# Performance work log

Hardware: AMD Instinct MI355X
Metric: run time of the kernel (lower is better)

## Reference

```python
import jax, jax.numpy as jnp
import numpy as np

B, NPTS = 2, 60000
NX, NY = 256, 256
PCR0, PCR1 = -32.0, -32.0
PS0, PS1 = 0.25, 0.25
MAXPP = 32      # max points per pillar
MAXP = 12000    # max pillars
C = 64          # lidar_channels
SENT = NX * NY  # sentinel pillar id (> any valid id)
NEG = -1e9
EPS = 1e-5


def setup_inputs():
    key = jax.random.key(0)
    ks = jax.random.split(key, 16)
    xy = jax.random.uniform(ks[0], (B, NPTS, 2), minval=-34.0, maxval=34.0)
    z = jax.random.uniform(ks[1], (B, NPTS, 1), minval=-3.0, maxval=1.0)
    ir = jax.random.uniform(ks[2], (B, NPTS, 2))
    pts = jnp.concatenate([xy, z, ir], axis=-1).astype(jnp.float32)
    mask = jax.random.uniform(ks[3], (B, NPTS)) < 0.98

    def lin(k, i, o):
        return (jax.random.normal(k, (i, o)) / np.sqrt(i)).astype(jnp.float32)

    inp = {"lidar_points": pts, "lidar_mask": mask,
           "w1": lin(ks[4], 10, 64), "b1": 0.01 * jax.random.normal(ks[5], (64,), jnp.float32),
           "g1": jnp.ones(64, jnp.float32), "be1": jnp.zeros(64, jnp.float32),
           "w2": lin(ks[6], 64, 64), "b2": 0.01 * jax.random.normal(ks[7], (64,), jnp.float32),
           "g2": jnp.ones(64, jnp.float32), "be2": jnp.zeros(64, jnp.float32)}
    for i, n in enumerate(["1", "2", "3"]):
        inp["cw" + n] = (jax.random.normal(ks[8 + i], (64, 64, 3, 3)) / np.sqrt(64 * 9)).astype(jnp.float32)
        inp["cb" + n] = 0.01 * jax.random.normal(ks[11 + i], (64,), jnp.float32)
        inp["cg" + n] = jnp.ones(64, jnp.float32)
        inp["cbe" + n] = jnp.zeros(64, jnp.float32)
    return inp


def bn1d(x, g, b):  # training-mode BN over rows (biased var), matches torch BatchNorm1d forward
    m = x.mean(0)
    v = ((x - m) ** 2).mean(0)
    return (x - m) * jax.lax.rsqrt(v + EPS) * g + b


def bn2d(x, g, b):  # training-mode BN over (N,H,W) per channel
    m = x.mean((0, 2, 3), keepdims=True)
    v = ((x - m) ** 2).mean((0, 2, 3), keepdims=True)
    return (x - m) * jax.lax.rsqrt(v + EPS) * g[None, :, None, None] + b[None, :, None, None]


def conv3(x, w, b):
    y = jax.lax.conv_general_dilated(x, w, (1, 1), 'SAME',
                                     dimension_numbers=('NCHW', 'OIHW', 'NCHW'))
    return y + b[None, :, None, None]


def pillarize(pts, msk):
    """pts: (N,5) xyzir, msk: (N,) bool -> padded pillar tensors (fixed shapes)."""
    n = pts.shape[0]
    ix = jnp.clip(((pts[:, 0] - PCR0) / PS0).astype(jnp.int32), 0, NX - 1)
    iy = jnp.clip(((pts[:, 1] - PCR1) / PS1).astype(jnp.int32), 0, NY - 1)
    pid = jnp.where(msk, iy * NX + ix, SENT)
    # sorted unique ids; keep the first (smallest) MAXP, like torch.unique + truncation
    spid = jnp.sort(pid)
    is_new = jnp.concatenate([jnp.array([True]), spid[1:] != spid[:-1]])
    urank = jnp.cumsum(is_new) - 1
    dest = jnp.where(is_new & (urank < MAXP) & (spid < SENT), urank, MAXP)
    uids = jnp.full((MAXP + 1,), SENT, dtype=pid.dtype).at[dest].set(spid)[:MAXP]  # ascending, SENT-padded
    inv = jnp.clip(jnp.searchsorted(uids, pid), 0, MAXP - 1)
    valid = (uids[inv] == pid) & (pid < SENT)
    # rank of each point within its pillar, in original point order (stable sort)
    seg = jnp.where(valid, inv, MAXP)
    order = jnp.argsort(seg)  # stable
    sseg = seg[order]
    pos = jnp.arange(n)
    first = jnp.concatenate([jnp.array([True]), sseg[1:] != sseg[:-1]])
    start = jax.lax.cummax(jnp.where(first, pos, 0))
    rank = jnp.zeros(n, jnp.int32).at[order].set((pos - start).astype(jnp.int32))
    keep = valid & (rank < MAXPP)  # first MAXPP points per pillar (matches truncation-then-mean)
    seg2 = jnp.where(keep, inv, MAXP)  # dump slot = MAXP
    cnt = jnp.zeros(MAXP + 1, pts.dtype).at[seg2].add(1.0)
    sums = jnp.zeros((MAXP + 1, 3), pts.dtype).at[seg2].add(jnp.where(keep[:, None], pts[:, :3], 0.0))
    mean = sums / jnp.maximum(cnt, 1.0)[:, None]
    ctr = mean[seg2]  # per-point pillar centroid (over kept points)
    gx = PCR0 + ((pid % NX).astype(pts.dtype) + 0.5) * PS0
    gy = PCR1 + ((pid // NX).astype(pts.dtype) + 0.5) * PS1
    aug = jnp.concatenate([pts, pts[:, :3] - ctr, gx[:, None], gy[:, None]], axis=1)  # (N,10)
    rk = jnp.minimum(rank, MAXPP - 1)
    pf = jnp.zeros((MAXP + 1, MAXPP, 10), pts.dtype).at[seg2, rk].set(
        jnp.where(keep[:, None], aug, 0.0))[:MAXP]
    pm = jnp.zeros((MAXP + 1, MAXPP), bool).at[seg2, rk].set(keep)[:MAXP]
    pvalid = uids < SENT
    coords = jnp.where(pvalid[:, None], jnp.stack([uids % NX, uids // NX], axis=-1), 0)
    return pf, pm, coords, pvalid


def pillar_net(pf, pm, w1, b1, g1, be1, w2, b2, g2, be2):
    npil, pp, ci = pf.shape
    x = pf.reshape(npil * pp, ci) @ w1 + b1
    x = jax.nn.relu(bn1d(x, g1, be1))
    x = x @ w2 + b2
    x = jax.nn.relu(bn1d(x, g2, be2))
    x = x.reshape(npil, pp, -1)
    x = jnp.where(pm[:, :, None], x, NEG)
    return x.max(axis=1)  # (npil, C)


def reference(lidar_points, lidar_mask, w1, b1, g1, be1, w2, b2, g2, be2,
              cw1, cb1, cg1, cbe1, cw2, cb2, cg2, cbe2, cw3, cb3, cg3, cbe3):
    pf, pm, coords, pvalid = jax.vmap(pillarize)(lidar_points, lidar_mask)
    # pillar net is applied per batch element in the original loop -> per-sample BN stats
    feat = jax.vmap(lambda a, m: pillar_net(a, m, w1, b1, g1, be1, w2, b2, g2, be2))(pf, pm)
    lin = coords[..., 1] * NX + coords[..., 0]          # (B, MAXP)
    f = jnp.where(pvalid[..., None], feat, 0.0)          # padded pillars contribute nothing
    bev = jax.vmap(lambda l, ff: jnp.zeros((NY * NX, C), ff.dtype).at[l].add(ff))(lin, f)
    bev = bev.reshape(-1, NY, NX, C).transpose(0, 3, 1, 2)  # (B,C,NY,NX)
    x = jax.nn.relu(bn2d(conv3(bev, cw1, cb1), cg1, cbe1))
    x = jax.nn.relu(bn2d(conv3(x, cw2, cb2), cg2, cbe2))
    x = jax.nn.relu(bn2d(conv3(x, cw3, cb3), cg3, cbe3))
    return x
```

## Files before the change

kernel.cpp:

```cpp
#include <hip/hip_runtime.h>

#define NPTS 60000
#define NXG 256
#define NCELL 65536
#define MAXP 12000
#define MAXPP 32
#define NROWS (MAXP*MAXPP)

typedef float f32x32 __attribute__((ext_vector_type(32)));
typedef float f32x4  __attribute__((ext_vector_type(4)));
typedef short s16x8  __attribute__((ext_vector_type(8)));

__device__ __forceinline__ short to_bf16(float f){
  unsigned u = __float_as_uint(f);
  unsigned r = (u + 0x7FFFu + ((u>>16)&1u)) >> 16;
  return (short)r;
}
__device__ __forceinline__ float rl(float v, int c){
  return __int_as_float(__builtin_amdgcn_readlane(__float_as_int(v), c));
}

__global__ __launch_bounds__(256) void prep(uint4* __restrict__ p1, size_t n1,
                                            uint4* __restrict__ p2, size_t n2,
                                            const float* __restrict__ w0, const float* __restrict__ w1,
                                            const float* __restrict__ w2, short* __restrict__ wh){
  size_t idx = (size_t)blockIdx.x*256 + threadIdx.x;
  size_t stride = (size_t)gridDim.x*256;
  const uint4 z = make_uint4(0,0,0,0);
  for (size_t k=idx; k<n1; k+=stride) p1[k]=z;
  for (size_t k=idx; k<n2; k+=stride) p2[k]=z;
  for (size_t k=idx; k<3*36864; k+=stride){
    int l = (int)(k / 36864), r = (int)(k - (size_t)l*36864);
    const float* w = (l==0)? w0 : ((l==1)? w1 : w2);
    int ic = r & 63, oc = (r>>6)&63, tap = r>>12;
    wh[k] = to_bf16(w[(oc*64+ic)*9 + tap]);
  }
}

__global__ void compute_pid(const float* __restrict__ pts, const void* __restrict__ maskp,
                            int* __restrict__ pid, int* __restrict__ pptr,
                            int* __restrict__ ccnt){
  __shared__ int cf32, cbig;
  if (threadIdx.x==0){ cf32=0; cbig=0; }
  __syncthreads();
  {
    int lf=0, lb=0;
    const unsigned* mu = (const unsigned*)maskp;
    for (int k=0;k<4;k++){
      unsigned x = mu[threadIdx.x*4+k];
      if (x==0x3f800000u) lf++;
      else if (x>1u) lb++;
    }
    if (lf) atomicAdd(&cf32, lf);
    if (lb) atomicAdd(&cbig, lb);
  }
  __syncthreads();
  int mode = (cf32>64) ? 2 : ((cbig>0) ? 1 : 0);
  int i = blockIdx.x*blockDim.x + threadIdx.x;
  if (i>=NPTS) return;
  int b = blockIdx.y;
  int gi = b*NPTS+i;
  bool m;
  if (mode==0)      m = ((const int*)maskp)[gi]!=0;
  else if (mode==1) m = ((const unsigned char*)maskp)[gi]!=0;
  else              m = ((const float*)maskp)[gi]!=0.f;
  int cell = -1;
  if (m){
    float x = pts[(size_t)gi*5+0], y = pts[(size_t)gi*5+1];
    int ix = (int)((x - (-32.0f)) / 0.25f);
    ix = ix<0?0:(ix>255?255:ix);
    int iy = (int)((y - (-32.0f)) / 0.25f);
    iy = iy<0?0:(iy>255?255:iy);
    cell = iy*NXG + ix;
    atomicAdd(&ccnt[b*NCELL+cell], 1);
  }
  pid[gi] = cell;
  pptr[gi] = -1;
}

__global__ __launch_bounds__(256) void scan_a(const int* __restrict__ ccnt,
                                              int2* __restrict__ bpart){
  int b = blockIdx.y, blk = blockIdx.x, t = threadIdx.x;
  int4 v = *(const int4*)&ccnt[b*NCELL + blk*1024 + t*4];
  int occ = (v.x>0)+(v.y>0)+(v.z>0)+(v.w>0);
  int cnt = v.x+v.y+v.z+v.w;
  #pragma unroll
  for (int off=32; off>0; off>>=1){
    occ += __shfl_xor(occ, off, 64);
    cnt += __shfl_xor(cnt, off, 64);
  }
  __shared__ int so[4], sc[4];
  int wv = t>>6, lane = t&63;
  if (lane==0){ so[wv]=occ; sc[wv]=cnt; }
  __syncthreads();
  if (t==0) bpart[b*64+blk] = make_int2(so[0]+so[1]+so[2]+so[3], sc[0]+sc[1]+sc[2]+sc[3]);
}

__global__ __launch_bounds__(256) void scan_b(const int* __restrict__ ccnt,
    const int2* __restrict__ bpart,
    int* __restrict__ crank, int* __restrict__ cstart, int* __restrict__ pcell,
    int* __restrict__ misc, int* __restrict__ heavy){
  __shared__ int swo[4], swc[4], sk[4];
  __shared__ int bo_, bc_;
  int b = blockIdx.y, blk = blockIdx.x, t = threadIdx.x;
  int wv = t>>6, lane = t&63;
  if (t < 64){
    int2 p = bpart[b*64+t];
    int po = (t<blk)? p.x : 0;
    int pc = (t<blk)? p.y : 0;
    int to = p.x;
    int tc = p.y;
    #pragma unroll
    for (int off=32; off>0; off>>=1){
      po += __shfl_xor(po, off, 64);
      pc += __shfl_xor(pc, off, 64);
      to += __shfl_xor(to, off, 64);
      tc += __shfl_xor(tc, off, 64);
    }
    if (t==0){
      bo_ = po; bc_ = pc;
      if (blk==0){
        misc[1+b] = (to < MAXP) ? to : MAXP;
        misc[5+b] = tc;
      }
    }
  }
  int4 v = *(const int4*)&ccnt[b*NCELL + blk*1024 + t*4];
  int occ = (v.x>0)+(v.y>0)+(v.z>0)+(v.w>0);
  int cnt = v.x+v.y+v.z+v.w;
  int io = occ, ic = cnt;
  #pragma unroll
  for (int off=1; off<64; off<<=1){
    int ao = __shfl_up(io, off, 64);
    int ac = __shfl_up(ic, off, 64);
    if (lane >= off){ io += ao; ic += ac; }
  }
  if (lane==63){ swo[wv]=io; swc[wv]=ic; }
  __syncthreads();
  int wvo=0, wvc=0;
  #pragma unroll
  for (int w2=0; w2<4; w2++){
    if (w2<wv){ wvo += swo[w2]; wvc += swc[w2]; }
  }
  int eo = bo_ + wvo + io - occ;
  int ec = bc_ + wvc + ic - cnt;
  int kept = 0;
  int cellb = blk*1024 + t*4;
  int vv[4] = {v.x,v.y,v.z,v.w};
  #pragma unroll
  for (int j=0;j<4;j++){
    int c = cellb+j; int val = vv[j];
    if (val>0){
      crank[b*NCELL+c]=eo; cstart[b*NCELL+c]=ec;
      if (eo<MAXP){
        pcell[b*MAXP+eo]=c;
        kept += (val<MAXPP)? val : MAXPP;
        if (val>MAXPP){
          int hi = atomicAdd(&heavy[b],1);
          if (hi<64) heavy[2 + b*64 + hi] = c;
        }
      }
      eo++; ec+=val;
    }
  }
  #pragma unroll
  for (int off=32; off>0; off>>=1) kept += __shfl_xor(kept, off, 64);
  if (lane==0) sk[wv]=kept;
  __syncthreads();
  if (t==0) atomicAdd(&misc[3+b], sk[0]+sk[1]+sk[2]+sk[3]);
}

__global__ void scatter_points(const int* __restrict__ pid, const int* __restrict__ ccnt,
    const int* __restrict__ crank, const int* __restrict__ cstart,
    int* __restrict__ ctmp, int* __restrict__ plist, int* __restrict__ pptr){
  int i = blockIdx.x*blockDim.x + threadIdx.x;
  if (i>=NPTS) return;
  int b = blockIdx.y;
  int gi = b*NPTS+i;
  int cell = pid[gi];
  if (cell<0) return;
  int bc = b*NCELL+cell;
  int pos = cstart[bc] + atomicAdd(&ctmp[bc],1);
  plist[b*NPTS+pos] = i;
  int r = crank[bc];
  if (r>=0 && r<MAXP && ccnt[bc]<=MAXPP) pptr[gi] = r;
}

__global__ void heavy_select(const int* __restrict__ ccnt, const int* __restrict__ crank,
    const int* __restrict__ cstart, const int* __restrict__ plist,
    const int* __restrict__ heavy, int* __restrict__ pptr){
  int b = blockIdx.y;
  int hn = heavy[b]; if (hn>64) hn=64;
  if ((int)blockIdx.x >= hn) return;
  int cell = heavy[2 + b*64 + blockIdx.x];
  int bc = b*NCELL+cell;
  int cnt = ccnt[bc], start = cstart[bc], pr = crank[bc];
  for (int e=threadIdx.x; e<cnt; e+=blockDim.x){
    int pe = plist[b*NPTS+start+e];
    int rank=0;
    for (int k=0;k<cnt;k++) rank += (plist[b*NPTS+start+k] < pe);
    if (rank<MAXPP) pptr[b*NPTS+pe] = pr;
  }
}

__global__ __launch_bounds__(256) void gather_cpts(const float* __restrict__ pts,
    const int* __restrict__ pid, const int* __restrict__ pptr,
    const int* __restrict__ plist, const int* __restrict__ misc,
    float* __restrict__ cpts, float* __restrict__ psum){
  int pos = blockIdx.x*256 + threadIdx.x;
  int b = blockIdx.y;
  if (pos >= misc[5+b]) return;
  int i = plist[b*NPTS+pos];
  int gi = b*NPTS+i;
  const float* qp = &pts[(size_t)gi*5];
  float x=qp[0], y=qp[1], z=qp[2], i1=qp[3], i2=qp[4];
  int cell = pid[gi];
  int rid = pptr[gi];
  float gx = -32.0f + ((float)(cell&255)+0.5f)*0.25f;
  float gy = -32.0f + ((float)(cell>>8)+0.5f)*0.25f;
  float4* cp = (float4*)&cpts[(size_t)(b*NPTS+pos)*8];
  cp[0] = make_float4(x,y,z,i1);
  cp[1] = make_float4(i2,gx,gy,__int_as_float(rid));
  if (rid>=0){
    float* s = &psum[(size_t)(b*MAXP+rid)*4];
    atomicAdd(s+0,x); atomicAdd(s+1,y); atomicAdd(s+2,z); atomicAdd(s+3,1.f);
  }
}

#define MM_ACC(K,V) { if ((K)<32) m0[(K)&31]+=(V); else if ((K)<64) m1[((K)-32)&31]+=(V); else m2+=(V); }
__global__ __launch_bounds__(256) void moments(const float* __restrict__ cpts,
    const float* __restrict__ psum, const int* __restrict__ misc,
    float* __restrict__ lstat){
  int b = blockIdx.y;
  int n = misc[5+b];
  f32x32 m0, m1; float m2 = 0.f;
  #pragma unroll
  for (int j=0;j<32;j++){ m0[j]=0.f; m1[j]=0.f; }
  for (int pos = blockIdx.x*256+threadIdx.x; pos<n; pos += gridDim.x*256){
    const float4* cp = (const float4*)&cpts[(size_t)(b*NPTS+pos)*8];
    float4 f1 = cp[0], f2 = cp[1];
    int rid = __float_as_int(f2.w);
    if (rid<0) continue;
    float4 mc = *(const float4*)&psum[(size_t)(b*MAXP+rid)*4];
    float inv = 1.f/fmaxf(mc.w,1.f);
    float aug[10] = {f1.x,f1.y,f1.z,f1.w,f2.x,
                     f1.x-mc.x*inv, f1.y-mc.y*inv, f1.z-mc.z*inv, f2.y, f2.z};
    #pragma unroll
    for (int d=0; d<10; d++){
      #pragma unroll
      for (int e=d; e<10; e++){
        const int k = d*10 - d*(d-1)/2 + (e-d);
        MM_ACC(k, aug[d]*aug[e]);
      }
      const int kl = 55+d;
      MM_ACC(kl, aug[d]);
    }
  }
  int lane = threadIdx.x & 63;
  int rep = ((blockIdx.x*256+threadIdx.x)>>6) & 15;
  float* dst = &lstat[(size_t)(rep*2+b)*65];
  #pragma unroll
  for (int j=0;j<32;j++){
    float v = m0[j];
    #pragma unroll
    for (int off=32; off>0; off>>=1) v += __shfl_xor(v, off, 64);
    if (lane==0) atomicAdd(&dst[j], v);
  }
  #pragma unroll
  for (int j=0;j<32;j++){
    float v = m1[j];
    #pragma unroll
    for (int off=32; off>0; off>>=1) v += __shfl_xor(v, off, 64);
    if (lane==0) atomicAdd(&dst[32+j], v);
  }
  {
    float v = m2;
    #pragma unroll
    for (int off=32; off>0; off>>=1) v += __shfl_xor(v, off, 64);
    if (lane==0) atomicAdd(&dst[64], v);
  }
}

__global__ __launch_bounds__(256) void pillar_mlp(const float* __restrict__ cpts,
    const int* __restrict__ pcell, const int* __restrict__ cstart,
    const int* __restrict__ ccnt, const float* __restrict__ psum,
    const int* __restrict__ misc,
    const float* __restrict__ w1, const float* __restrict__ b1,
    const float* __restrict__ g1, const float* __restrict__ be1,
    const float* __restrict__ w2, const float* __restrict__ b2,
    const float* __restrict__ lstat, float* __restrict__ l2stat,
    float* __restrict__ fmx, float* __restrict__ fmn){
  __shared__ float sM[2][65];
  const int lane = threadIdx.x & 63;
  float w1c[10];
  #pragma unroll
  for (int d=0;d<10;d++) w1c[d] = w1[d*64+lane];
  for (int e=threadIdx.x; e<130; e+=256){
    int bb = e/65, k = e-bb*65;
    float s=0.f;
    for (int r=0;r<16;r++) s += lstat[(size_t)(r*2+bb)*65+k];
    sM[bb][k]=s;
  }
  __syncthreads();
  const float b1c = b1[lane], b2c = b2[lane];
  const float g1c = g1[lane], be1c = be1[lane];
  float sc1_0, sh1_0, sc1_1, sh1_1;
  #pragma unroll
  for (int bb=0;bb<2;bb++){
    float nk = (float)misc[3+bb];
    const float N = (float)NROWS;
    float pad = N - nk;
    float lw = 0.f;
    #pragma unroll
    for (int d=0;d<10;d++) lw += sM[bb][55+d]*w1c[d];
    float s = nk*b1c + lw;
    float qq = nk*b1c*b1c + 2.f*b1c*lw;
    #pragma unroll
    for (int d=0; d<10; d++){
      #pragma unroll
      for (int e=d; e<10; e++){
        float m = sM[bb][d*10 - d*(d-1)/2 + (e-d)];
        qq += ((d==e)?1.f:2.f)*m*w1c[d]*w1c[e];
      }
    }
    float St = s + pad*b1c;
    float Qt = qq + pad*b1c*b1c;
    float mu = St/N;
    float var = fmaxf(Qt/N - mu*mu, 0.f);
    float sc = g1c*rsqrtf(var+1e-5f);
    float sh = be1c-mu*sc;
    if (bb){ sc1_1=sc; sh1_1=sh; } else { sc1_0=sc; sh1_0=sh; }
  }
  f32x32 w2lo, w2hi;
  #pragma unroll
  for (int c=0;c<32;c++) w2lo[c] = w2[(size_t)c*64+lane];
  #pragma unroll
  for (int c=0;c<32;c++) w2hi[c] = w2[(size_t)(c+32)*64+lane];
  const int npil0 = misc[1], npil1 = misc[2];
  float s2_0=0.f, q2_0=0.f, s2_1=0.f, q2_1=0.f;

  const int wglobal = (blockIdx.x*256 + threadIdx.x) >> 6;
  const int nwaves = (gridDim.x*256) >> 6;
  for (int qq = wglobal; qq < 2*MAXP; qq += nwaves){
    int b = (qq >= MAXP) ? 1 : 0;
    int p = qq - b*MAXP;
    int npil = b ? npil1 : npil0;
    if (p >= npil) continue;
    int cell = pcell[b*MAXP+p];
    int bc = b*NCELL+cell;
    int cnt = ccnt[bc], start = cstart[bc];
    const float* mc = &psum[(size_t)(b*MAXP+p)*4];
    float minv = 1.f/fmaxf(mc[3],1.f);
    float mx = mc[0]*minv, my = mc[1]*minv, mz = mc[2]*minv;
    float gx = -32.0f + ((float)(cell&255)+0.5f)*0.25f;
    float gy = -32.0f + ((float)(cell>>8)+0.5f)*0.25f;
    float sc1 = b ? sc1_1 : sc1_0;
    float sh1 = b ? sh1_1 : sh1_0;
    float tmax = -1e30f, tmin = 1e30f;
    float s2 = 0.f, q2 = 0.f;
    const float4* cpb = (const float4*)&cpts[(size_t)(b*NPTS+start)*8];
    float4 f1 = cpb[0], f2 = cpb[1];
    for (int k=0; k<cnt; k++){
      float4 nf1, nf2;
      if (k+1 < cnt){ nf1 = cpb[2*(k+1)]; nf2 = cpb[2*(k+1)+1]; }
      int rid = __float_as_int(f2.w);
      if (rid == p){
        float x=f1.x, y=f1.y, z=f1.z, i1=f1.w, i2=f2.x;
        float acc = b1c;
        acc = fmaf(x, w1c[0], acc);
        acc = fmaf(y, w1c[1], acc);
        acc = fmaf(z, w1c[2], acc);
        acc = fmaf(i1, w1c[3], acc);
        acc = fmaf(i2, w1c[4], acc);
        acc = fmaf(x-mx, w1c[5], acc);
        acc = fmaf(y-my, w1c[6], acc);
        acc = fmaf(z-mz, w1c[7], acc);
        acc = fmaf(gx, w1c[8], acc);
        acc = fmaf(gy, w1c[9], acc);
        float zz = fmaxf(acc*sc1+sh1, 0.f);
        float t0 = b2c, t1 = 0.f, t2c = 0.f, t3 = 0.f;
        #pragma unroll
        for (int c=0;c<16;c++){
          t0  = fmaf(rl(zz,c),    w2lo[c],    t0);
          t1  = fmaf(rl(zz,c+16), w2lo[c+16], t1);
          t2c = fmaf(rl(zz,c+32), w2hi[c],    t2c);
          t3  = fmaf(rl(zz,c+48), w2hi[c+16], t3);
        }
        float t = (t0+t1)+(t2c+t3);
        tmax = fmaxf(tmax, t);
        tmin = fminf(tmin, t);
        s2 += t; q2 += t*t;
      }
      f1 = nf1; f2 = nf2;
    }
    fmx[(size_t)(b*MAXP+p)*64 + lane] = tmax;
    fmn[(size_t)(b*MAXP+p)*64 + lane] = tmin;
    if (b){ s2_1 += s2; q2_1 += q2; } else { s2_0 += s2; q2_0 += q2; }
  }
  int rep = wglobal & 15;
  atomicAdd(&l2stat[((rep*2+0)*2+0)*64+lane], s2_0);
  atomicAdd(&l2stat[((rep*2+0)*2+1)*64+lane], q2_0);
  atomicAdd(&l2stat[((rep*2+1)*2+0)*64+lane], s2_1);
  atomicAdd(&l2stat[((rep*2+1)*2+1)*64+lane], q2_1);
}

__global__ void stats_fin2(const float* __restrict__ w1, const float* __restrict__ b1,
    const float* __restrict__ g1, const float* __restrict__ be1,
    const float* __restrict__ w2, const float* __restrict__ b2,
    const float* __restrict__ g2, const float* __restrict__ be2,
    const float* __restrict__ lstat, const float* __restrict__ l2stat,
    const int* __restrict__ misc, float* __restrict__ stats){
  __shared__ float M[65];
  __shared__ float z0s[64];
  int b = blockIdx.x, c = threadIdx.x;
  for (int e=c; e<65; e+=64){
    float s=0.f;
    for (int r=0;r<16;r++) s += lstat[(size_t)(r*2+b)*65+e];
    M[e]=s;
  }
  __syncthreads();
  float wcol[10];
  #pragma unroll
  for (int d=0;d<10;d++) wcol[d] = w1[d*64+c];
  float b1c = b1[c];
  float nk = (float)misc[3+b];
  const float N = (float)NROWS;
  float pad = N - nk;
  float lw = 0.f;
  #pragma unroll
  for (int d=0;d<10;d++) lw += M[55+d]*wcol[d];
  float s = nk*b1c + lw;
  float qq = nk*b1c*b1c + 2.f*b1c*lw;
  #pragma unroll
  for (int d=0; d<10; d++){
    #pragma unroll
    for (int e=d; e<10; e++){
      float m = M[d*10 - d*(d-1)/2 + (e-d)];
      qq += ((d==e)?1.f:2.f)*m*wcol[d]*wcol[e];
    }
  }
  float St = s + pad*b1c;
  float Qt = qq + pad*b1c*b1c;
  float mu = St/N;
  float var = fmaxf(Qt/N - mu*mu, 0.f);
  float sc1 = g1[c]*rsqrtf(var+1e-5f);
  float sh1 = be1[c]-mu*sc1;
  float z0 = fmaxf(b1c*sc1+sh1, 0.f);
  z0s[c]=z0;
  __syncthreads();
  float t0 = b2[c];
  for (int i2=0;i2<64;i2++) t0 += z0s[i2]*w2[(size_t)i2*64+c];
  float s2 = pad*t0, q2 = pad*t0*t0;
  for (int r=0;r<16;r++){
    s2 += l2stat[((r*2+b)*2+0)*64+c];
    q2 += l2stat[((r*2+b)*2+1)*64+c];
  }
  float m2 = s2/N;
  float v2 = fmaxf(q2/N - m2*m2, 0.f);
  float sc2 = g2[c]*rsqrtf(v2+1e-5f);
  float* S = &stats[(size_t)b*512];
  S[384+c]=sc2; S[448+c]=be2[c]-m2*sc2;
}

__global__ void scatter_bev(const float* __restrict__ fmx, const float* __restrict__ fmn,
                            const int* __restrict__ pcell, const int* __restrict__ misc,
                            const float* __restrict__ stats, short* __restrict__ bevh){
  int tid = blockIdx.x*256+threadIdx.x;
  if (tid >= 2*64*MAXP) return;
  int c = tid & 63;
  int bp = tid >> 6;
  int b = bp / MAXP;
  int p = bp - b*MAXP;
  if (p >= misc[1+b]) return;
  float sc2 = stats[(size_t)b*512+384+c], sh2 = stats[(size_t)b*512+448+c];
  float t = (sc2 >= 0.f) ? fmx[tid] : fmn[tid];
  float v = fmaxf(sc2*t+sh2, 0.f);
  int cell = pcell[b*MAXP+p];
  bevh[((size_t)((b<<16) + cell))*64 + c] = to_bf16(v);
}

#define MFMA16(A,B,C) __builtin_amdgcn_mfma_f32_16x16x32_bf16(A,B,C,0,0,0)

__global__ __launch_bounds__(512,4) void conv_mfma(const short* __restrict__ xh,
    const short* __restrict__ wh, const float* __restrict__ bias,
    const float* __restrict__ pstat, const float* __restrict__ pg, const float* __restrict__ pbe,
    short* __restrict__ outh, float* __restrict__ outf,
    float* __restrict__ stat){
  __shared__ short sX[324*40];
  __shared__ short sW[576*40];
  __shared__ float sBN[128];
  __shared__ float ss[64], sq[64];
  const int tX = blockIdx.x*16, tY = blockIdx.y*16;
  const int b = blockIdx.z;
  const int t = threadIdx.x;
  const int lane = t & 63, wv = t >> 6;
  const int colx = lane & 15;
  const int kb = (lane >> 4) * 8;
  const int ocb = (wv >> 2) * 32;
  const int ry  = (wv & 3) * 4;
  if (t < 64){ ss[t]=0.f; sq[t]=0.f; }
  if (t >= 64 && t < 128 && pstat){
    int c = t-64;
    const float n = 131072.f;
    float m = pstat[c]/n;
    float v = fmaxf(pstat[64+c]/n - m*m, 0.f);
    float sc = pg[c]*rsqrtf(v+1e-5f);
    sBN[c]=sc; sBN[64+c]=pbe[c]-m*sc;
  }

  f32x4 a00={0.f,0.f,0.f,0.f}, a01=a00, a02=a00, a03=a00;
  f32x4 a10=a00, a11=a00, a12=a00, a13=a00;

  for (int h=0; h<2; ++h){
    __syncthreads();
    for (int e=t; e<1296; e+=512){
      int px = e>>2, j = e&3;
      int yy = px/18, xx = px - yy*18;
      int gy = tY+yy-1, gx = tX+xx-1;
      uint4 v = make_uint4(0,0,0,0);
      if ((unsigned)gy<256u && (unsigned)gx<256u){
        v = *(const uint4*)&xh[((size_t)((b<<16) + (gy<<8) + gx))*64 + h*32 + j*8];
        if (pstat){
          unsigned arr[4] = {v.x, v.y, v.z, v.w};
          #pragma unroll
          for (int j2=0;j2<4;j2++){
            unsigned wrd = arr[j2];
            int ch = h*32 + j*8 + j2*2;
            float lo = __uint_as_float(wrd<<16);
            float hi = __uint_as_float(wrd & 0xffff0000u);
            lo = fmaxf(lo*sBN[ch]+sBN[64+ch], 0.f);
            hi = fmaxf(hi*sBN[ch+1]+sBN[64+ch+1], 0.f);
            arr[j2] = (unsigned)(unsigned short)to_bf16(lo) |
                      (((unsigned)(unsigned short)to_bf16(hi))<<16);
          }
          v = make_uint4(arr[0],arr[1],arr[2],arr[3]);
        }
      }
      *(uint4*)&sX[px*40 + j*8] = v;
    }
    for (int e=t; e<2304; e+=512){
      int row = e>>2, j = e&3;
      int tap = row>>6, oc = row&63;
      uint4 v = *(const uint4*)&wh[(size_t)tap*4096 + oc*64 + h*32 + j*8];
      *(uint4*)&sW[row*40 + j*8] = v;
    }
    __syncthreads();
    #pragma unroll
    for (int tap=0; tap<9; ++tap){
      const int dy = tap/3, dx = tap - dy*3;
      s16x8 wA = *(const s16x8*)&sW[(tap*64 + ocb +  0 + colx)*40 + kb];
      s16x8 wB = *(const s16x8*)&sW[(tap*64 + ocb + 16 + colx)*40 + kb];
      s16x8 x0 = *(const s16x8*)&sX[((ry+0+dy)*18 + colx+dx)*40 + kb];
      s16x8 x1 = *(const s16x8*)&sX[((ry+1+dy)*18 + colx+dx)*40 + kb];
      s16x8 x2 = *(const s16x8*)&sX[((ry+2+dy)*18 + colx+dx)*40 + kb];
      s16x8 x3 = *(const s16x8*)&sX[((ry+3+dy)*18 + colx+dx)*40 + kb];
      a00 = MFMA16(wA,x0,a00); a01 = MFMA16(wA,x1,a01);
      a02 = MFMA16(wA,x2,a02); a03 = MFMA16(wA,x3,a03);
      a10 = MFMA16(wB,x0,a10); a11 = MFMA16(wB,x1,a11);
      a12 = MFMA16(wB,x2,a12); a13 = MFMA16(wB,x3,a13);
    }
  }
  const int ocl = (lane>>4)*4;
  #define DOG(G, A0,A1,A2,A3) { \
    const int oc0g = ocb + G*16 + ocl; \
    float bj0=bias[oc0g], bj1=bias[oc0g+1], bj2=bias[oc0g+2], bj3=bias[oc0g+3]; \
    float v00=A0[0]+bj0, v01=A0[1]+bj1, v02=A0[2]+bj2, v03=A0[3]+bj3; \
    float v10=A1[0]+bj0, v11=A1[1]+bj1, v12=A1[2]+bj2, v13=A1[3]+bj3; \
    float v20=A2[0]+bj0, v21=A2[1]+bj1, v22=A2[2]+bj2, v23=A2[3]+bj3; \
    float v30=A3[0]+bj0, v31=A3[1]+bj1, v32=A3[2]+bj2, v33=A3[3]+bj3; \
    float s0=v00+v10+v20+v30, q0=v00*v00+v10*v10+v20*v20+v30*v30; \
    float s1=v01+v11+v21+v31, q1=v01*v01+v11*v11+v21*v21+v31*v31; \
    float s2=v02+v12+v22+v32, q2=v02*v02+v12*v12+v22*v22+v32*v32; \
    float s3=v03+v13+v23+v33, q3=v03*v03+v13*v13+v23*v23+v33*v33; \
    s0+=__shfl_xor(s0,1,64); s0+=__shfl_xor(s0,2,64); s0+=__shfl_xor(s0,4,64); s0+=__shfl_xor(s0,8,64); \
    q0+=__shfl_xor(q0,1,64); q0+=__shfl_xor(q0,2,64); q0+=__shfl_xor(q0,4,64); q0+=__shfl_xor(q0,8,64); \
    s1+=__shfl_xor(s1,1,64); s1+=__shfl_xor(s1,2,64); s1+=__shfl_xor(s1,4,64); s1+=__shfl_xor(s1,8,64); \
    q1+=__shfl_xor(q1,1,64); q1+=__shfl_xor(q1,2,64); q1+=__shfl_xor(q1,4,64); q1+=__shfl_xor(q1,8,64); \
    s2+=__shfl_xor(s2,1,64); s2+=__shfl_xor(s2,2,64); s2+=__shfl_xor(s2,4,64); s2+=__shfl_xor(s2,8,64); \
    q2+=__shfl_xor(q2,1,64); q2+=__shfl_xor(q2,2,64); q2+=__shfl_xor(q2,4,64); q2+=__shfl_xor(q2,8,64); \
    s3+=__shfl_xor(s3,1,64); s3+=__shfl_xor(s3,2,64); s3+=__shfl_xor(s3,4,64); s3+=__shfl_xor(s3,8,64); \
    q3+=__shfl_xor(q3,1,64); q3+=__shfl_xor(q3,2,64); q3+=__shfl_xor(q3,4,64); q3+=__shfl_xor(q3,8,64); \
    if (colx==0){ \
      atomicAdd(&ss[oc0g],s0);   atomicAdd(&sq[oc0g],q0); \
      atomicAdd(&ss[oc0g+1],s1); atomicAdd(&sq[oc0g+1],q1); \
      atomicAdd(&ss[oc0g+2],s2); atomicAdd(&sq[oc0g+2],q2); \
      atomicAdd(&ss[oc0g+3],s3); atomicAdd(&sq[oc0g+3],q3); \
    } \
    if (outh){ \
      size_t pb = (size_t)((b<<16) + tX + colx); \
      *(short4*)&outh[(pb + ((tY+ry+0)<<8))*64 + oc0g] = make_short4(to_bf16(v00),to_bf16(v01),to_bf16(v02),to_bf16(v03)); \
      *(short4*)&outh[(pb + ((tY+ry+1)<<8))*64 + oc0g] = make_short4(to_bf16(v10),to_bf16(v11),to_bf16(v12),to_bf16(v13)); \
      *(short4*)&outh[(pb + ((tY+ry+2)<<8))*64 + oc0g] = make_short4(to_bf16(v20),to_bf16(v21),to_bf16(v22),to_bf16(v23)); \
      *(short4*)&outh[(pb + ((tY+ry+3)<<8))*64 + oc0g] = make_short4(to_bf16(v30),to_bf16(v31),to_bf16(v32),to_bf16(v33)); \
    } else { \
      size_t cb0 = (((size_t)(b*64+oc0g))<<16) + ((tY+ry)<<8) + tX + colx; \
      outf[cb0          ] = v00; outf[cb0+(1<<16)      ] = v01; outf[cb0+(2<<16)      ] = v02; outf[cb0+(3<<16)      ] = v03; \
      outf[cb0+256      ] = v10; outf[cb0+(1<<16)+256  ] = v11; outf[cb0+(2<<16)+256  ] = v12; outf[cb0+(3<<16)+256  ] = v13; \
      outf[cb0+512      ] = v20; outf[cb0+(1<<16)+512  ] = v21; outf[cb0+(2<<16)+512  ] = v22; outf[cb0+(3<<16)+512  ] = v23; \
      outf[cb0+768      ] = v30; outf[cb0+(1<<16)+768  ] = v31; outf[cb0+(2<<16)+768  ] = v32; outf[cb0+(3<<16)+768  ] = v33; \
    } \
  }
  DOG(0, a00,a01,a02,a03)
  DOG(1, a10,a11,a12,a13)
  #undef DOG
  __syncthreads();
  if (t < 64){
    atomicAdd(&stat[t],    ss[t]);
    atomicAdd(&stat[64+t], sq[t]);
  }
}

__global__ __launch_bounds__(256) void bn_apply(float* __restrict__ x, const float* __restrict__ bnst,
                                                const float* __restrict__ g, const float* __restrict__ be){
  __shared__ float sBN[128];
  if (threadIdx.x < 64){
    int c = threadIdx.x;
    const float n = 131072.f;
    float m = bnst[c]/n;
    float v = fmaxf(bnst[64+c]/n - m*m, 0.f);
    float sc = g[c]*rsqrtf(v+1e-5f);
    sBN[c]=sc; sBN[64+c]=be[c]-m*sc;
  }
  __syncthreads();
  size_t idx = (size_t)blockIdx.x*256 + threadIdx.x;
  size_t stride = (size_t)gridDim.x*256;
  float4* p = (float4*)x;
  for (size_t k=idx; k<2097152ULL; k+=stride){
    int c = (int)((k>>14)&63);
    float sc = sBN[c], sh = sBN[64+c];
    float4 v = p[k];
    v.x=fmaxf(v.x*sc+sh,0.f); v.y=fmaxf(v.y*sc+sh,0.f);
    v.z=fmaxf(v.z*sc+sh,0.f); v.w=fmaxf(v.w*sc+sh,0.f);
    p[k]=v;
  }
}

extern "C" void kernel_launch(void* const* d_in, const int* in_sizes, int n_in,
                              void* d_out, int out_size, void* d_ws, size_t ws_size,
                              hipStream_t stream){
  const float* pts  = (const float*)d_in[0];
  const void*  mask = d_in[1];
  const float* w1 = (const float*)d_in[2];
  const float* b1 = (const float*)d_in[3];
  const float* g1 = (const float*)d_in[4];
  const float* be1= (const float*)d_in[5];
  const float* w2 = (const float*)d_in[6];
  const float* b2 = (const float*)d_in[7];
  const float* g2 = (const float*)d_in[8];
  const float* be2= (const float*)d_in[9];
  const float* cw[3]  = {(const float*)d_in[10],(const float*)d_in[14],(const float*)d_in[18]};
  const float* cb[3]  = {(const float*)d_in[11],(const float*)d_in[15],(const float*)d_in[19]};
  const float* cg[3]  = {(const float*)d_in[12],(const float*)d_in[16],(const float*)d_in[20]};
  const float* cbe[3] = {(const float*)d_in[13],(const float*)d_in[17],(const float*)d_in[21]};
  float* out = (float*)d_out;

  char* W = (char*)d_ws;
  size_t off = 0;
  auto A = [&](size_t n){ size_t r = off; off = (off + n + 255) & ~(size_t)255; return r; };
  short*    BIGH  = (short*)   (W + A((size_t)2*NCELL*64*2));
  short*    OUT1H = (short*)   (W + A((size_t)2*NCELL*64*2));
  int*      PID   = (int*)     (W + A((size_t)2*NPTS*4));
  int*      CRANK = (int*)     (W + A((size_t)2*NCELL*4));
  int*      CSTART= (int*)     (W + A((size_t)2*NCELL*4));
  int*      PLIST = (int*)     (W + A((size_t)2*NPTS*4));
  int*      PPTR  = (int*)     (W + A((size_t)2*NPTS*4));
  int*      PCELL = (int*)     (W + A((size_t)2*MAXP*4));
  float*    CPTS  = (float*)   (W + A((size_t)2*NPTS*8*4));
  float*    FMX   = (float*)   (W + A((size_t)2*MAXP*64*4));
  float*    FMN   = (float*)   (W + A((size_t)2*MAXP*64*4));
  short*    WH    = (short*)   (W + A((size_t)3*36864*2));
  int2*     BPART = (int2*)    (W + A((size_t)2*64*8));
  size_t zbeg = off;
  int*      CCNT  = (int*)     (W + A((size_t)2*NCELL*4));
  int*      CTMP  = (int*)     (W + A((size_t)2*NCELL*4));
  float*    PSUM  = (float*)   (W + A((size_t)2*MAXP*16));
  float*    STATS = (float*)   (W + A((size_t)2*512*4));
  float*    LSTAT = (float*)   (W + A((size_t)16*2*65*4));
  float*    L2STAT= (float*)   (W + A((size_t)16*2*2*64*4));
  float*    BNST  = (float*)   (W + A((size_t)3*256*4));
  int*      HEAVY = (int*)     (W + A((size_t)(2+2*64)*4));
  int*      MISC  = (int*)     (W + A(256));
  size_t zend = off;

  prep<<<2048,256,0,stream>>>((uint4*)BIGH, (size_t)2*NCELL*64*2/16,
                              (uint4*)(W+zbeg), (zend-zbeg)/16,
                              cw[0], cw[1], cw[2], WH);

  dim3 perPt((NPTS+255)/256, 2);

  compute_pid<<<perPt,256,0,stream>>>(pts, mask, PID, PPTR, CCNT);
  scan_a<<<dim3(64,2),256,0,stream>>>(CCNT, BPART);
  scan_b<<<dim3(64,2),256,0,stream>>>(CCNT, BPART, CRANK, CSTART, PCELL, MISC, HEAVY);
  scatter_points<<<perPt,256,0,stream>>>(PID, CCNT, CRANK, CSTART, CTMP, PLIST, PPTR);
  heavy_select<<<dim3(64,2),64,0,stream>>>(CCNT, CRANK, CSTART, PLIST, HEAVY, PPTR);
  gather_cpts<<<perPt,256,0,stream>>>(pts, PID, PPTR, PLIST, MISC, CPTS, PSUM);
  moments<<<dim3(120,2),256,0,stream>>>(CPTS, PSUM, MISC, LSTAT);
  pillar_mlp<<<2048,256,0,stream>>>(CPTS, PCELL, CSTART, CCNT, PSUM, MISC,
                                    w1, b1, g1, be1, w2, b2, LSTAT, L2STAT, FMX, FMN);
  stats_fin2<<<2,64,0,stream>>>(w1, b1, g1, be1, w2, b2, g2, be2, LSTAT, L2STAT, MISC, STATS);
  scatter_bev<<<(2*64*MAXP+255)/256,256,0,stream>>>(FMX, FMN, PCELL, MISC, STATS, BIGH);

  conv_mfma<<<dim3(16,16,2),512,0,stream>>>(BIGH, WH, cb[0], nullptr, nullptr, nullptr,
                                            OUT1H, nullptr, BNST);
  conv_mfma<<<dim3(16,16,2),512,0,stream>>>(OUT1H, WH+36864, cb[1], BNST, cg[0], cbe[0],
                                            BIGH, nullptr, BNST+256);
  conv_mfma<<<dim3(16,16,2),512,0,stream>>>(BIGH, WH+2*36864, cb[2], BNST+256, cg[1], cbe[1],
                                            nullptr, out, BNST+512);
  bn_apply<<<2048,256,0,stream>>>(out, BNST+512, cg[2], cbe[2]);
}
```

Measured before the change: 217.6 us.

## Give each wave a contiguous pillar range and cache centroid offsets in point records

The moments kernel now writes each point's offset from its pillar mean into a widened 12-float point record, so pillar_mlp no longer reads psum. pillar_mlp is launched with a batch grid dimension, and each wave streams through a contiguous range of pillars' points, flushing max/min whenever the pillar id changes. Previously each wave handled one pillar at a time with per-pillar setup. The aim is to cut per-pillar overhead and improve load balance. The cost is extra point-record bandwidth and a possible imbalance when pillar point counts are uneven.

```diff
diff --git a/kernel.cpp b/kernel.cpp
--- a/kernel.cpp
+++ b/kernel.cpp
@@ -218,7 +218,7 @@
   int rid = pptr[gi];
   float gx = -32.0f + ((float)(cell&255)+0.5f)*0.25f;
   float gy = -32.0f + ((float)(cell>>8)+0.5f)*0.25f;
-  float4* cp = (float4*)&cpts[(size_t)(b*NPTS+pos)*8];
+  float4* cp = (float4*)&cpts[(size_t)(b*NPTS+pos)*12];
   cp[0] = make_float4(x,y,z,i1);
   cp[1] = make_float4(i2,gx,gy,__int_as_float(rid));
   if (rid>=0){
@@ -228,7 +228,7 @@
 }
 
 #define MM_ACC(K,V) { if ((K)<32) m0[(K)&31]+=(V); else if ((K)<64) m1[((K)-32)&31]+=(V); else m2+=(V); }
-__global__ __launch_bounds__(256) void moments(const float* __restrict__ cpts,
+__global__ __launch_bounds__(256) void moments(float* __restrict__ cpts,
     const float* __restrict__ psum, const int* __restrict__ misc,
     float* __restrict__ lstat){
   int b = blockIdx.y;
@@ -237,14 +237,15 @@
   #pragma unroll
   for (int j=0;j<32;j++){ m0[j]=0.f; m1[j]=0.f; }
   for (int pos = blockIdx.x*256+threadIdx.x; pos<n; pos += gridDim.x*256){
-    const float4* cp = (const float4*)&cpts[(size_t)(b*NPTS+pos)*8];
+    float4* cp = (float4*)&cpts[(size_t)(b*NPTS+pos)*12];
     float4 f1 = cp[0], f2 = cp[1];
     int rid = __float_as_int(f2.w);
     if (rid<0) continue;
     float4 mc = *(const float4*)&psum[(size_t)(b*MAXP+rid)*4];
     float inv = 1.f/fmaxf(mc.w,1.f);
-    float aug[10] = {f1.x,f1.y,f1.z,f1.w,f2.x,
-                     f1.x-mc.x*inv, f1.y-mc.y*inv, f1.z-mc.z*inv, f2.y, f2.z};
+    float dx = f1.x-mc.x*inv, dy = f1.y-mc.y*inv, dz = f1.z-mc.z*inv;
+    cp[2] = make_float4(dx,dy,dz,0.f);
+    float aug[10] = {f1.x,f1.y,f1.z,f1.w,f2.x, dx,dy,dz, f2.y,f2.z};
     #pragma unroll
     for (int d=0; d<10; d++){
       #pragma unroll
@@ -283,43 +284,40 @@
 
 __global__ __launch_bounds__(256) void pillar_mlp(const float* __restrict__ cpts,
     const int* __restrict__ pcell, const int* __restrict__ cstart,
-    const int* __restrict__ ccnt, const float* __restrict__ psum,
-    const int* __restrict__ misc,
+    const int* __restrict__ ccnt, const int* __restrict__ misc,
     const float* __restrict__ w1, const float* __restrict__ b1,
     const float* __restrict__ g1, const float* __restrict__ be1,
     const float* __restrict__ w2, const float* __restrict__ b2,
     const float* __restrict__ lstat, float* __restrict__ l2stat,
     float* __restrict__ fmx, float* __restrict__ fmn){
-  __shared__ float sM[2][65];
+  __shared__ float sM[65];
+  const int b = blockIdx.y;
   const int lane = threadIdx.x & 63;
   float w1c[10];
   #pragma unroll
   for (int d=0;d<10;d++) w1c[d] = w1[d*64+lane];
-  for (int e=threadIdx.x; e<130; e+=256){
-    int bb = e/65, k = e-bb*65;
+  for (int e=threadIdx.x; e<65; e+=256){
     float s=0.f;
-    for (int r=0;r<16;r++) s += lstat[(size_t)(r*2+bb)*65+k];
-    sM[bb][k]=s;
+    for (int r=0;r<16;r++) s += lstat[(size_t)(r*2+b)*65+e];
+    sM[e]=s;
   }
   __syncthreads();
   const float b1c = b1[lane], b2c = b2[lane];
-  const float g1c = g1[lane], be1c = be1[lane];
-  float sc1_0, sh1_0, sc1_1, sh1_1;
-  #pragma unroll
-  for (int bb=0;bb<2;bb++){
-    float nk = (float)misc[3+bb];
+  float sc1, sh1;
+  {
+    float nk = (float)misc[3+b];
     const float N = (float)NROWS;
     float pad = N - nk;
     float lw = 0.f;
     #pragma unroll
-    for (int d=0;d<10;d++) lw += sM[bb][55+d]*w1c[d];
+    for (int d=0;d<10;d++) lw += sM[55+d]*w1c[d];
     float s = nk*b1c + lw;
     float qq = nk*b1c*b1c + 2.f*b1c*lw;
     #pragma unroll
     for (int d=0; d<10; d++){
       #pragma unroll
       for (int e=d; e<10; e++){
-        float m = sM[bb][d*10 - d*(d-1)/2 + (e-d)];
+        float m = sM[d*10 - d*(d-1)/2 + (e-d)];
         qq += ((d==e)?1.f:2.f)*m*w1c[d]*w1c[e];
       }
     }
@@ -327,81 +325,82 @@
     float Qt = qq + pad*b1c*b1c;
     float mu = St/N;
     float var = fmaxf(Qt/N - mu*mu, 0.f);
-    float sc = g1c*rsqrtf(var+1e-5f);
-    float sh = be1c-mu*sc;
-    if (bb){ sc1_1=sc; sh1_1=sh; } else { sc1_0=sc; sh1_0=sh; }
+    sc1 = g1[lane]*rsqrtf(var+1e-5f);
+    sh1 = be1[lane]-mu*sc1;
   }
   f32x32 w2lo, w2hi;
   #pragma unroll
   for (int c=0;c<32;c++) w2lo[c] = w2[(size_t)c*64+lane];
   #pragma unroll
   for (int c=0;c<32;c++) w2hi[c] = w2[(size_t)(c+32)*64+lane];
-  const int npil0 = misc[1], npil1 = misc[2];
-  float s2_0=0.f, q2_0=0.f, s2_1=0.f, q2_1=0.f;
-
-  const int wglobal = (blockIdx.x*256 + threadIdx.x) >> 6;
-  const int nwaves = (gridDim.x*256) >> 6;
-  for (int qq = wglobal; qq < 2*MAXP; qq += nwaves){
-    int b = (qq >= MAXP) ? 1 : 0;
-    int p = qq - b*MAXP;
-    int npil = b ? npil1 : npil0;
-    if (p >= npil) continue;
-    int cell = pcell[b*MAXP+p];
-    int bc = b*NCELL+cell;
-    int cnt = ccnt[bc], start = cstart[bc];
-    const float* mc = &psum[(size_t)(b*MAXP+p)*4];
-    float minv = 1.f/fmaxf(mc[3],1.f);
-    float mx = mc[0]*minv, my = mc[1]*minv, mz = mc[2]*minv;
-    float gx = -32.0f + ((float)(cell&255)+0.5f)*0.25f;
-    float gy = -32.0f + ((float)(cell>>8)+0.5f)*0.25f;
-    float sc1 = b ? sc1_1 : sc1_0;
-    float sh1 = b ? sh1_1 : sh1_0;
+  const int npil = misc[1+b];
+  const int w = blockIdx.x*4 + (threadIdx.x>>6);
+  const int nw = gridDim.x*4;
+  float s2 = 0.f, q2 = 0.f;
+  const int ppw = (npil + nw - 1)/nw;
+  int p0 = w*ppw;
+  if (npil > 0 && p0 < npil){
+    int p1 = p0+ppw; if (p1>npil) p1=npil;
+    int c0 = pcell[b*MAXP+p0];
+    int cl = pcell[b*MAXP+p1-1];
+    int start = cstart[b*NCELL+c0];
+    int end = cstart[b*NCELL+cl] + ccnt[b*NCELL+cl];
+    int cur = -1;
     float tmax = -1e30f, tmin = 1e30f;
-    float s2 = 0.f, q2 = 0.f;
-    const float4* cpb = (const float4*)&cpts[(size_t)(b*NPTS+start)*8];
-    float4 f1 = cpb[0], f2 = cpb[1];
-    for (int k=0; k<cnt; k++){
-      float4 nf1, nf2;
-      if (k+1 < cnt){ nf1 = cpb[2*(k+1)]; nf2 = cpb[2*(k+1)+1]; }
-      int rid = __float_as_int(f2.w);
-      if (rid == p){
-        float x=f1.x, y=f1.y, z=f1.z, i1=f1.w, i2=f2.x;
+    const float4* cpb = (const float4*)&cpts[(size_t)b*NPTS*12];
+    float4 a0 = cpb[(size_t)start*3+0];
+    float4 a1 = cpb[(size_t)start*3+1];
+    float4 a2 = cpb[(size_t)start*3+2];
+    for (int pos=start; pos<end; ++pos){
+      float4 n0, n1, n2;
+      if (pos+1 < end){
+        size_t nb = (size_t)(pos+1)*3;
+        n0 = cpb[nb]; n1 = cpb[nb+1]; n2 = cpb[nb+2];
+      }
+      int rid = __float_as_int(a1.w);
+      if (rid >= 0){
+        if (rid != cur){
+          if (cur >= 0){
+            fmx[(size_t)(b*MAXP+cur)*64 + lane] = tmax;
+            fmn[(size_t)(b*MAXP+cur)*64 + lane] = tmin;
+          }
+          cur = rid; tmax = -1e30f; tmin = 1e30f;
+        }
         float acc = b1c;
-        acc = fmaf(x, w1c[0], acc);
-        acc = fmaf(y, w1c[1], acc);
-        acc = fmaf(z, w1c[2], acc);
-        acc = fmaf(i1, w1c[3], acc);
-        acc = fmaf(i2, w1c[4], acc);
-        acc = fmaf(x-mx, w1c[5], acc);
-        acc = fmaf(y-my, w1c[6], acc);
-        acc = fmaf(z-mz, w1c[7], acc);
-        acc = fmaf(gx, w1c[8], acc);
-        acc = fmaf(gy, w1c[9], acc);
+        acc = fmaf(a0.x, w1c[0], acc);
+        acc = fmaf(a0.y, w1c[1], acc);
+        acc = fmaf(a0.z, w1c[2], acc);
+        acc = fmaf(a0.w, w1c[3], acc);
+        acc = fmaf(a1.x, w1c[4], acc);
+        acc = fmaf(a2.x, w1c[5], acc);
+        acc = fmaf(a2.y, w1c[6], acc);
+        acc = fmaf(a2.z, w1c[7], acc);
+        acc = fmaf(a1.y, w1c[8], acc);
+        acc = fmaf(a1.z, w1c[9], acc);
         float zz = fmaxf(acc*sc1+sh1, 0.f);
-        float t0 = b2c, t1 = 0.f, t2c = 0.f, t3 = 0.f;
+        float t0 = b2c, t1 = 0.f, t2v = 0.f, t3 = 0.f;
         #pragma unroll
         for (int c=0;c<16;c++){
           t0  = fmaf(rl(zz,c),    w2lo[c],    t0);
           t1  = fmaf(rl(zz,c+16), w2lo[c+16], t1);
-          t2c = fmaf(rl(zz,c+32), w2hi[c],    t2c);
+          t2v = fmaf(rl(zz,c+32), w2hi[c],    t2v);
           t3  = fmaf(rl(zz,c+48), w2hi[c+16], t3);
         }
-        float t = (t0+t1)+(t2c+t3);
+        float t = (t0+t1)+(t2v+t3);
         tmax = fmaxf(tmax, t);
         tmin = fminf(tmin, t);
         s2 += t; q2 += t*t;
       }
-      f1 = nf1; f2 = nf2;
-    }
-    fmx[(size_t)(b*MAXP+p)*64 + lane] = tmax;
-    fmn[(size_t)(b*MAXP+p)*64 + lane] = tmin;
-    if (b){ s2_1 += s2; q2_1 += q2; } else { s2_0 += s2; q2_0 += q2; }
-  }
-  int rep = wglobal & 15;
-  atomicAdd(&l2stat[((rep*2+0)*2+0)*64+lane], s2_0);
-  atomicAdd(&l2stat[((rep*2+0)*2+1)*64+lane], q2_0);
-  atomicAdd(&l2stat[((rep*2+1)*2+0)*64+lane], s2_1);
-  atomicAdd(&l2stat[((rep*2+1)*2+1)*64+lane], q2_1);
+      a0=n0; a1=n1; a2=n2;
+    }
+    if (cur >= 0){
+      fmx[(size_t)(b*MAXP+cur)*64 + lane] = tmax;
+      fmn[(size_t)(b*MAXP+cur)*64 + lane] = tmin;
+    }
+  }
+  int rep = w & 15;
+  atomicAdd(&l2stat[((rep*2+b)*2+0)*64+lane], s2);
+  atomicAdd(&l2stat[((rep*2+b)*2+1)*64+lane], q2);
 }
 
 __global__ void stats_fin2(const float* __restrict__ w1, const float* __restrict__ b1,
@@ -665,7 +664,7 @@
   int*      PLIST = (int*)     (W + A((size_t)2*NPTS*4));
   int*      PPTR  = (int*)     (W + A((size_t)2*NPTS*4));
   int*      PCELL = (int*)     (W + A((size_t)2*MAXP*4));
-  float*    CPTS  = (float*)   (W + A((size_t)2*NPTS*8*4));
+  float*    CPTS  = (float*)   (W + A((size_t)2*NPTS*12*4));
   float*    FMX   = (float*)   (W + A((size_t)2*MAXP*64*4));
   float*    FMN   = (float*)   (W + A((size_t)2*MAXP*64*4));
   short*    WH    = (short*)   (W + A((size_t)3*36864*2));
@@ -695,8 +694,8 @@
   heavy_select<<<dim3(64,2),64,0,stream>>>(CCNT, CRANK, CSTART, PLIST, HEAVY, PPTR);
   gather_cpts<<<perPt,256,0,stream>>>(pts, PID, PPTR, PLIST, MISC, CPTS, PSUM);
   moments<<<dim3(120,2),256,0,stream>>>(CPTS, PSUM, MISC, LSTAT);
-  pillar_mlp<<<2048,256,0,stream>>>(CPTS, PCELL, CSTART, CCNT, PSUM, MISC,
-                                    w1, b1, g1, be1, w2, b2, LSTAT, L2STAT, FMX, FMN);
+  pillar_mlp<<<dim3(1024,2),256,0,stream>>>(CPTS, PCELL, CSTART, CCNT, MISC,
+                                            w1, b1, g1, be1, w2, b2, LSTAT, L2STAT, FMX, FMN);
   stats_fin2<<<2,64,0,stream>>>(w1, b1, g1, be1, w2, b2, g2, be2, LSTAT, L2STAT, MISC, STATS);
   scatter_bev<<<(2*64*MAXP+255)/256,256,0,stream>>>(FMX, FMN, PCELL, MISC, STATS, BIGH);
 
```

Result: no change. 220.8 us, median of 2 (+1.5%).
